# Kernel optimization log

Measured on AMD Instinct MI355X. Metric: run time of the kernel, lower is better.

Reference implementation:

```python
import jax, jax.numpy as jnp
import numpy as np

DIM = 768
HEADS = 12
HEAD_DIM = DIM // HEADS
SCALE = HEAD_DIM ** -0.5
EPS = 1e-6


def setup_inputs() -> dict:
    key = jax.random.key(0)
    ks = jax.random.split(key, 10)
    B, Nq, Nk, C = 4, 4096, 4096, DIM
    std = C ** -0.5
    return {
        "x_q": jax.random.normal(ks[0], (B, Nq, C), jnp.float32),
        "x_kv": jax.random.normal(ks[1], (B, Nk, C), jnp.float32),
        "Wq": jax.random.normal(ks[2], (C, C), jnp.float32) * std,
        "bq": jnp.zeros((C,), jnp.float32),
        "Wk": jax.random.normal(ks[3], (C, C), jnp.float32) * std,
        "bk": jnp.zeros((C,), jnp.float32),
        "Wv": jax.random.normal(ks[4], (C, C), jnp.float32) * std,
        "bv": jnp.zeros((C,), jnp.float32),
        "Wp": jax.random.normal(ks[5], (C, C), jnp.float32) * std,
        "bp": jnp.zeros((C,), jnp.float32),
    }


def _phi(x):
    # ELU(alpha=1) + 1 positive feature map
    return jax.nn.elu(x) + 1.0


def reference(x_q, x_kv, Wq, bq, Wk, bk, Wv, bv, Wp, bp):
    B, Nq, C = x_q.shape
    Nk = x_kv.shape[1]
    h, d = HEADS, HEAD_DIM
    # projections (torch Linear: x @ W.T + b)
    q = x_q @ Wq.T + bq   # [B,Nq,C]
    k = x_kv @ Wk.T + bk  # [B,Nk,C]
    v = x_kv @ Wv.T + bv  # [B,Nk,C]
    # split heads -> [B,h,N,d]
    q = q.reshape(B, Nq, h, d).transpose(0, 2, 1, 3) * SCALE
    k = k.reshape(B, Nk, h, d).transpose(0, 2, 1, 3)
    v = v.reshape(B, Nk, h, d).transpose(0, 2, 1, 3)
    q_phi = _phi(q)
    k_phi = _phi(k)
    # KV state [B,h,d,d] and normalizer sum [B,h,d]
    kv = jnp.einsum('bhnd,bhne->bhde', k_phi, v)
    k_sum = k_phi.sum(axis=2)
    out = jnp.einsum('bhnd,bhde->bhne', q_phi, kv)
    z = jnp.einsum('bhnd,bhd->bhn', q_phi, k_sum)[..., None] + EPS
    out = out / z
    out = out.transpose(0, 2, 1, 3).reshape(B, Nq, C)
    return out @ Wp.T + bp
```

## Files before the change

### kernel.cpp

```cpp
#include <hip/hip_runtime.h>
#include <hip/hip_bf16.h>
#include <cstdint>
#include <cstddef>

#define HD_B   4
#define SEQ    4096
#define CDIM   768
#define HEADS  12
#define HDIM   64
#define MROWS  (HD_B * SEQ)
#define QSCALE 0.125f
#define EPSV   1e-6f

typedef __attribute__((ext_vector_type(8))) short  short8v;
typedef __attribute__((ext_vector_type(4))) float  f32x4;

__device__ __forceinline__ unsigned short f2b(float f) {
    unsigned int u = __float_as_uint(f);
    u += 0x7FFFu + ((u >> 16) & 1u);
    return (unsigned short)(u >> 16);
}
__device__ __forceinline__ float b2f(unsigned short b) {
    return __uint_as_float(((unsigned int)b) << 16);
}
__device__ __forceinline__ float phi_f(float x) {
    return x > 0.f ? x + 1.f : __expf(x);
}

#define GLOAD_LDS16(g, l)                                             \
    __builtin_amdgcn_global_load_lds(                                 \
        (__attribute__((address_space(1))) void*)(void*)(g),          \
        (__attribute__((address_space(3))) void*)(l), 16, 0, 0)

#define VMW12() asm volatile("s_waitcnt vmcnt(12)" ::: "memory")
#define VMW4()  asm volatile("s_waitcnt vmcnt(4)"  ::: "memory")
#define VMW0()  asm volatile("s_waitcnt vmcnt(0)"  ::: "memory")
#define LGW()   asm volatile("s_waitcnt lgkmcnt(0)" ::: "memory")
#define SB()    do { __builtin_amdgcn_sched_barrier(0);               \
                     __builtin_amdgcn_s_barrier();                    \
                     __builtin_amdgcn_sched_barrier(0); } while (0)

__global__ void wcvt_all(const float* __restrict__ wq, const float* __restrict__ wk,
                         const float* __restrict__ wv, const float* __restrict__ wp,
                         unsigned short* __restrict__ dst) {
    const int y = blockIdx.y;
    const float* src = (y == 0) ? wq : (y == 1) ? wk : (y == 2) ? wv : wp;
    const int i = blockIdx.x * 256 + threadIdx.x;
    float4 v = reinterpret_cast<const float4*>(src)[i];
    ushort4 o;
    o.x = f2b(v.x); o.y = f2b(v.y); o.z = f2b(v.z); o.w = f2b(v.w);
    reinterpret_cast<ushort4*>(dst + (size_t)y * (CDIM * CDIM))[i] = o;
}

template <int EPI, int NC>
__device__ __forceinline__ void proj_body(
    const float* __restrict__ A32,
    const unsigned short* __restrict__ Bp,
    const float* __restrict__ b0, const float* __restrict__ b1,
    unsigned short* __restrict__ o0, unsigned short* __restrict__ o1)
{
    constexpr int K  = CDIM;
    constexpr int T  = NC * 128;
    constexpr int NT = K / 64;

    __shared__ __align__(16) char smem[49152];
    char* As = smem;

    const int tid  = threadIdx.x;
    const int lane = tid & 63;
    const int w    = tid >> 6;
    const int wr   = w >> 1, wc = w & 1;

    const int bid  = blockIdx.x;
    const int s    = (bid & 7) * (T >> 3) + (bid >> 3);
    const int colp = s % NC;
    const int rowp = s / NC;
    const int brow = rowp * 128;
    const int bcol = colp * 128;

    const int r8  = lane >> 3;
    const int c8e = ((lane & 7) ^ r8) << 3;
    const int ar  = lane >> 4;
    const int ac  = (lane & 15) << 2;
    const int fr  = lane & 15;
    const int hi4 = lane >> 4;

    f32x4 acc[4][4];
#pragma unroll
    for (int i = 0; i < 4; ++i)
#pragma unroll
        for (int j = 0; j < 4; ++j)
            acc[i][j] = (f32x4){0.f, 0.f, 0.f, 0.f};

    auto stageB = [&](int buf, int kt) {
        char* dst = smem + 16384 + buf * 16384;
#pragma unroll
        for (int g = 0; g < 4; ++g) {
            const unsigned short* src =
                Bp + (size_t)(bcol + w * 32 + g * 8 + r8) * K + kt * 64 + c8e;
            GLOAD_LDS16(src, dst + (w * 32 + g * 8) * 128);
        }
    };

    float4 fA[8];
    auto aload = [&](int kt) {
#pragma unroll
        for (int j = 0; j < 8; ++j)
            fA[j] = *(const float4*)(A32 + (size_t)(brow + w * 32 + j * 4 + ar) * K
                                     + kt * 64 + ac);
    };
    auto awrite = [&]() {
#pragma unroll
        for (int j = 0; j < 8; ++j) {
            const int row = w * 32 + j * 4 + ar;
            unsigned int p0, p1;
            asm("v_cvt_pk_bf16_f32 %0, %1, %2" : "=v"(p0) : "v"(fA[j].x), "v"(fA[j].y));
            asm("v_cvt_pk_bf16_f32 %0, %1, %2" : "=v"(p1) : "v"(fA[j].z), "v"(fA[j].w));
            uint2 pk; pk.x = p0; pk.y = p1;
            *(uint2*)(As + row * 128 + ((ac << 1) ^ ((row & 7) << 4))) = pk;
        }
    };
    auto compute = [&](int bbuf) {
        const char* Bb = smem + 16384 + bbuf * 16384;
        short8v a[4][2];
#pragma unroll
        for (int i = 0; i < 4; ++i) {
            const int row = wr * 64 + i * 16 + fr;
#pragma unroll
            for (int ks = 0; ks < 2; ++ks)
                a[i][ks] = *(const short8v*)(As + row * 128 +
                              ((((ks << 2) + hi4) ^ (row & 7)) << 4));
        }
#pragma unroll
        for (int j = 0; j < 4; ++j) {
            const int row = wc * 64 + j * 16 + fr;
            short8v bb0 = *(const short8v*)(Bb + row * 128 + ((hi4 ^ (row & 7)) << 4));
            short8v bb1 = *(const short8v*)(Bb + row * 128 + (((4 + hi4) ^ (row & 7)) << 4));
#pragma unroll
            for (int i = 0; i < 4; ++i) {
                acc[i][j] = __builtin_amdgcn_mfma_f32_16x16x32_bf16(a[i][0], bb0, acc[i][j], 0, 0, 0);
                acc[i][j] = __builtin_amdgcn_mfma_f32_16x16x32_bf16(a[i][1], bb1, acc[i][j], 0, 0, 0);
            }
        }
    };

    aload(0);
    stageB(0, 0);
    VMW4();
    awrite();
    aload(1);
    stageB(1, 1);
    LGW();
    SB();

    for (int t = 0; t < NT; ++t) {
        const int c = t & 1;
        if (t == NT - 1) { VMW0(); } else { VMW12(); }
        SB();
        compute(c);
        SB();
        if (t < NT - 1) {
            VMW4();
            awrite();
            if (t < NT - 2) { aload(t + 2); stageB(c, t + 2); }
            LGW();
        }
    }

    float* ep = (float*)(void*)smem + w * (16 * 68);
    const int rr = lane >> 2;
    const int cb = (lane & 3) * 4;
    const bool isV = (EPI == 1) && (colp >= 6);
    const float* bptr = (EPI == 0) ? (b0 + bcol)
                        : (isV ? (b1 + (bcol - 768)) : (b0 + bcol));
    const int colbase = ((EPI == 1 && isV) ? bcol - 768 : bcol) + wc * 64;
    unsigned short* o16 = (EPI == 1 && isV) ? o1 : o0;

    float4 bb[4];
#pragma unroll
    for (int q = 0; q < 4; ++q)
        bb[q] = *(const float4*)&bptr[wc * 64 + q * 16 + cb];

#pragma unroll
    for (int i = 0; i < 4; ++i) {
#pragma unroll
        for (int j = 0; j < 4; ++j)
#pragma unroll
            for (int r = 0; r < 4; ++r)
                ep[(hi4 * 4 + r) * 68 + j * 16 + fr] = acc[i][j][r];
#pragma unroll
        for (int q = 0; q < 4; ++q) {
            const int cc = q * 16 + cb;
            f32x4 v = *(const f32x4*)&ep[rr * 68 + cc];
            const int rg = brow + wr * 64 + i * 16 + rr;
            const float4 bq = bb[q];
            ushort4 ov;
            if (EPI == 0) {
                ov.x = f2b(phi_f((v[0] + bq.x) * QSCALE));
                ov.y = f2b(phi_f((v[1] + bq.y) * QSCALE));
                ov.z = f2b(phi_f((v[2] + bq.z) * QSCALE));
                ov.w = f2b(phi_f((v[3] + bq.w) * QSCALE));
            } else if (!isV) {
                ov.x = f2b(phi_f(v[0] + bq.x));
                ov.y = f2b(phi_f(v[1] + bq.y));
                ov.z = f2b(phi_f(v[2] + bq.z));
                ov.w = f2b(phi_f(v[3] + bq.w));
            } else {
                ov.x = f2b(v[0] + bq.x);
                ov.y = f2b(v[1] + bq.y);
                ov.z = f2b(v[2] + bq.z);
                ov.w = f2b(v[3] + bq.w);
            }
            *(ushort4*)(o16 + (size_t)rg * 768 + (colbase + cc)) = ov;
        }
    }
}

__global__ __launch_bounds__(256, 3) void g_q(
    const float* __restrict__ xq, const unsigned short* __restrict__ wq,
    const float* __restrict__ bq, unsigned short* __restrict__ qphi)
{
    proj_body<0, 6>(xq, wq, bq, nullptr, qphi, nullptr);
}

__global__ __launch_bounds__(256, 3) void g_kv(
    const float* __restrict__ xkv, const unsigned short* __restrict__ wkv,
    const float* __restrict__ bk, const float* __restrict__ bv,
    unsigned short* __restrict__ kphi, unsigned short* __restrict__ v16)
{
    proj_body<1, 12>(xkv, wkv, bk, bv, kphi, v16);
}

__global__ __launch_bounds__(256) void g_out(
    const unsigned short* __restrict__ A16,
    const unsigned short* __restrict__ Bp,
    const float* __restrict__ bias,
    float* __restrict__ outp)
{
    constexpr int K = CDIM;
    __shared__ __align__(16) char smem[32768];
    char* As = smem;
    char* Bs = smem + 16384;

    const int tid  = threadIdx.x;
    const int lane = tid & 63;
    const int w    = tid >> 6;
    const int wr   = w >> 1, wc = w & 1;
    const int brow = blockIdx.x * 128;
    const int bcol = blockIdx.y * 128;

    const int r8  = lane >> 3;
    const int c8e = ((lane & 7) ^ r8) << 3;
    const int fr  = lane & 15;
    const int hi4 = lane >> 4;

    f32x4 acc[4][4];
#pragma unroll
    for (int i = 0; i < 4; ++i)
#pragma unroll
        for (int j = 0; j < 4; ++j)
            acc[i][j] = (f32x4){0.f, 0.f, 0.f, 0.f};

    for (int k0 = 0; k0 < K; k0 += 64) {
#pragma unroll
        for (int g = 0; g < 4; ++g) {
            const unsigned short* srcA =
                A16 + (size_t)(brow + w * 32 + g * 8 + r8) * K + k0 + c8e;
            GLOAD_LDS16(srcA, As + (w * 32 + g * 8) * 128);
            const unsigned short* srcB =
                Bp + (size_t)(bcol + w * 32 + g * 8 + r8) * K + k0 + c8e;
            GLOAD_LDS16(srcB, Bs + (w * 32 + g * 8) * 128);
        }
        __syncthreads();

        short8v a[4][2], b[4][2];
#pragma unroll
        for (int i = 0; i < 4; ++i) {
            const int row = wr * 64 + i * 16 + fr;
#pragma unroll
            for (int ks = 0; ks < 2; ++ks)
                a[i][ks] = *(const short8v*)(As + row * 128 +
                              ((((ks << 2) + hi4) ^ (row & 7)) << 4));
        }
#pragma unroll
        for (int j = 0; j < 4; ++j) {
            const int row = wc * 64 + j * 16 + fr;
#pragma unroll
            for (int ks = 0; ks < 2; ++ks)
                b[j][ks] = *(const short8v*)(Bs + row * 128 +
                              ((((ks << 2) + hi4) ^ (row & 7)) << 4));
        }
#pragma unroll
        for (int i = 0; i < 4; ++i)
#pragma unroll
            for (int j = 0; j < 4; ++j) {
                acc[i][j] = __builtin_amdgcn_mfma_f32_16x16x32_bf16(a[i][0], b[j][0], acc[i][j], 0, 0, 0);
                acc[i][j] = __builtin_amdgcn_mfma_f32_16x16x32_bf16(a[i][1], b[j][1], acc[i][j], 0, 0, 0);
            }
        __syncthreads();
    }

    float* ep = (float*)(void*)smem + w * (16 * 68);
    const int rr = lane >> 2;
    const int cb = (lane & 3) * 4;
    float4 bb[4];
#pragma unroll
    for (int q = 0; q < 4; ++q)
        bb[q] = *(const float4*)&bias[bcol + wc * 64 + q * 16 + cb];
#pragma unroll
    for (int i = 0; i < 4; ++i) {
#pragma unroll
        for (int j = 0; j < 4; ++j)
#pragma unroll
            for (int r = 0; r < 4; ++r)
                ep[(hi4 * 4 + r) * 68 + j * 16 + fr] = acc[i][j][r];
#pragma unroll
        for (int q = 0; q < 4; ++q) {
            const int cc = q * 16 + cb;
            f32x4 v = *(const f32x4*)&ep[rr * 68 + cc];
            const int rg = brow + wr * 64 + i * 16 + rr;
            const int cg = bcol + wc * 64 + cc;
            const float4 bq = bb[q];
            float4 ov;
            ov.x = v[0] + bq.x; ov.y = v[1] + bq.y;
            ov.z = v[2] + bq.z; ov.w = v[3] + bq.w;
            *(float4*)(outp + (size_t)rg * 768 + cg) = ov;
        }
    }
}

#define KVCH   128
#define KVITER 2
#define NCHUNK 16

__global__ __launch_bounds__(256, 3) void kv_part(
    const unsigned short* __restrict__ kphi,
    const unsigned short* __restrict__ vmat,
    float* __restrict__ part)
{
    const int bh = blockIdx.y;
    const int b  = bh / HEADS, h = bh % HEADS;
    const int c  = blockIdx.x;
    __shared__ unsigned short Kl[KVCH][HDIM];
    __shared__ float Vl[KVCH][HDIM];
    const int t  = threadIdx.x;
    const int i  = t >> 2;
    const int jb = t & 3;

    float acc[16];
#pragma unroll
    for (int jj = 0; jj < 16; ++jj) acc[jj] = 0.f;
    float ksum = 0.f;

    for (int it = 0; it < KVITER; ++it) {
        const size_t rbase = (size_t)b * SEQ + (size_t)c * (KVCH * KVITER) + it * KVCH;
        __syncthreads();
        for (int l = 0; l < KVCH / 32; ++l) {
            int row = l * 32 + (t >> 3);
            int col = (t & 7) << 3;
            const size_t g = (rbase + row) * CDIM + h * HDIM + col;
            int4 kk = *(const int4*)(kphi + g);
            int4 vv = *(const int4*)(vmat + g);
            *(int4*)&Kl[row][col] = kk;
            const unsigned short* vp = (const unsigned short*)&vv;
            float4 lo, hi;
            lo.x = b2f(vp[0]); lo.y = b2f(vp[1]); lo.z = b2f(vp[2]); lo.w = b2f(vp[3]);
            hi.x = b2f(vp[4]); hi.y = b2f(vp[5]); hi.z = b2f(vp[6]); hi.w = b2f(vp[7]);
            *(float4*)&Vl[row][col]     = lo;
            *(float4*)&Vl[row][col + 4] = hi;
        }
        __syncthreads();
        for (int n = 0; n < KVCH; ++n) {
            float kf = b2f(Kl[n][i]);
            const float4* vr = (const float4*)&Vl[n][jb * 16];
            float4 v0 = vr[0], v1 = vr[1], v2 = vr[2], v3 = vr[3];
            acc[0]  += kf * v0.x; acc[1]  += kf * v0.y; acc[2]  += kf * v0.z; acc[3]  += kf * v0.w;
            acc[4]  += kf * v1.x; acc[5]  += kf * v1.y; acc[6]  += kf * v1.z; acc[7]  += kf * v1.w;
            acc[8]  += kf * v2.x; acc[9]  += kf * v2.y; acc[10] += kf * v2.z; acc[11] += kf * v2.w;
            acc[12] += kf * v3.x; acc[13] += kf * v3.y; acc[14] += kf * v3.z; acc[15] += kf * v3.w;
            ksum += kf;
        }
    }
    float* op = part + ((size_t)c * 48 + bh) * 4160;
#pragma unroll
    for (int jj = 0; jj < 16; ++jj) op[i * 64 + jb * 16 + jj] = acc[jj];
    if (jb == 0) op[4096 + i] = ksum;
}

__global__ void kv_finalize(const float* __restrict__ part, float* __restrict__ kv) {
    int idx = blockIdx.x * 256 + threadIdx.x;
    if (idx >= 48 * 4160) return;
    float s = 0.f;
    for (int c = 0; c < NCHUNK; ++c) s += part[(size_t)c * 48 * 4160 + idx];
    kv[idx] = s;
}

__global__ __launch_bounds__(256) void attn_apply(
    const unsigned short* __restrict__ qphi,
    const float* __restrict__ kv,
    unsigned short* __restrict__ attn)
{
    const int h  = blockIdx.y;
    const int m0 = blockIdx.x * 64;
    const int b  = m0 >> 12;
    const int bh = b * HEADS + h;
    __shared__ float kvs[HDIM][HDIM];
    __shared__ float ksums[HDIM];
    __shared__ unsigned short ql[64][HDIM];
    const int t = threadIdx.x;
    const float* kvp = kv + (size_t)bh * 4160;
#pragma unroll
    for (int it = 0; it < 4; ++it) {
        int e = it * 1024 + t * 4;
        *(float4*)&kvs[e >> 6][e & 63] = *(const float4*)&kvp[e];
    }
    if (t < 64) ksums[t] = kvp[4096 + t];
#pragma unroll
    for (int it = 0; it < 2; ++it) {
        int row = it * 32 + (t >> 3);
        int col = (t & 7) << 3;
        *(int4*)&ql[row][col] =
            *(const int4*)(qphi + (size_t)(m0 + row) * CDIM + h * HDIM + col);
    }
    __syncthreads();

    const int r  = t >> 2;
    const int jb = t & 3;
    float acc[16];
#pragma unroll
    for (int jj = 0; jj < 16; ++jj) acc[jj] = 0.f;
    float z = 0.f;
    for (int q8 = 0; q8 < 8; ++q8) {
        short8v qv = *(const short8v*)&ql[r][q8 * 8];
#pragma unroll
        for (int dd = 0; dd < 8; ++dd) {
            float qd = b2f((unsigned short)qv[dd]);
            int d = q8 * 8 + dd;
            const float4* kr = (const float4*)&kvs[d][jb * 16];
            float4 k0 = kr[0], k1 = kr[1], k2 = kr[2], k3 = kr[3];
            acc[0]  += qd * k0.x; acc[1]  += qd * k0.y; acc[2]  += qd * k0.z; acc[3]  += qd * k0.w;
            acc[4]  += qd * k1.x; acc[5]  += qd * k1.y; acc[6]  += qd * k1.z; acc[7]  += qd * k1.w;
            acc[8]  += qd * k2.x; acc[9]  += qd * k2.y; acc[10] += qd * k2.z; acc[11] += qd * k2.w;
            acc[12] += qd * k3.x; acc[13] += qd * k3.y; acc[14] += qd * k3.z; acc[15] += qd * k3.w;
            z += qd * ksums[d];
        }
    }
    const float inv = 1.f / (z + EPSV);
    unsigned short* op = attn + (size_t)(m0 + r) * CDIM + h * HDIM + jb * 16;
#pragma unroll
    for (int jj = 0; jj < 16; ++jj) op[jj] = f2b(acc[jj] * inv);
}

extern "C" void kernel_launch(void* const* d_in, const int* in_sizes, int n_in,
                              void* d_out, int out_size, void* d_ws, size_t ws_size,
                              hipStream_t stream)
{
    const float* x_q  = (const float*)d_in[0];
    const float* x_kv = (const float*)d_in[1];
    const float* Wq   = (const float*)d_in[2];
    const float* bq   = (const float*)d_in[3];
    const float* Wk   = (const float*)d_in[4];
    const float* bk   = (const float*)d_in[5];
    const float* Wv   = (const float*)d_in[6];
    const float* bv   = (const float*)d_in[7];
    const float* Wp   = (const float*)d_in[8];
    const float* bp   = (const float*)d_in[9];
    float* out = (float*)d_out;

    char* ws = (char*)d_ws;
    size_t off = 0;
    auto alloc = [&](size_t bytes) -> char* {
        char* p = ws + off;
        off += (bytes + 255) & ~(size_t)255;
        return p;
    };
    const size_t xelems = (size_t)MROWS * CDIM;
    const size_t welems = (size_t)CDIM * CDIM;

    unsigned short* w16    = (unsigned short*)alloc(4 * welems * 2);
    unsigned short* wkv16  = w16 + welems;
    unsigned short* wp16   = w16 + 3 * welems;
    unsigned short* qphi   = (unsigned short*)alloc(xelems * 2);
    unsigned short* kphi   = (unsigned short*)alloc(xelems * 2);
    unsigned short* v16    = (unsigned short*)alloc(xelems * 2);
    unsigned short* attn16 = (unsigned short*)alloc(xelems * 2);
    float* part = (float*)alloc((size_t)NCHUNK * 48 * 4160 * 4);
    float* kvf  = (float*)alloc((size_t)48 * 4160 * 4);

    wcvt_all<<<dim3(576, 4), 256, 0, stream>>>(Wq, Wk, Wv, Wp, w16);

    g_q<<<768, 256, 0, stream>>>(x_q, w16, bq, qphi);

    g_kv<<<1536, 256, 0, stream>>>(x_kv, wkv16, bk, bv, kphi, v16);

    kv_part<<<dim3(NCHUNK, 48), 256, 0, stream>>>(kphi, v16, part);
    kv_finalize<<<(48 * 4160 + 255) / 256, 256, 0, stream>>>(part, kvf);
    attn_apply<<<dim3(MROWS / 64, HEADS), 256, 0, stream>>>(qphi, kvf, attn16);

    g_out<<<dim3(128, 6), 256, 0, stream>>>(attn16, wp16, bp, out);
}
```

Before: 214.0 us.

## Merge Q and KV projections into one launch and double-buffer output GEMM

The separate Q and KV projection kernels are replaced by one g_qkv kernel with 18 column tiles per row block, which picks the input, weight slice, bias and epilogue per tile from the column index. This removes a kernel launch and the tail between the two projections. The output projection GEMM gets a double-buffered LDS pipeline with global_load_lds prefetch two tiles ahead and vmcnt waits, instead of a load-sync-compute loop. It also gets the same bid-swizzled 1D grid mapping. LDS for g_out grows to 64KB, which may lower occupancy, and the merged kernel adds runtime branching on mode.

```diff
diff --git a/kernel.cpp b/kernel.cpp
--- a/kernel.cpp
+++ b/kernel.cpp
@@ -33,6 +33,7 @@
         (__attribute__((address_space(3))) void*)(l), 16, 0, 0)
 
 #define VMW12() asm volatile("s_waitcnt vmcnt(12)" ::: "memory")
+#define VMW8()  asm volatile("s_waitcnt vmcnt(8)"  ::: "memory")
 #define VMW4()  asm volatile("s_waitcnt vmcnt(4)"  ::: "memory")
 #define VMW0()  asm volatile("s_waitcnt vmcnt(0)"  ::: "memory")
 #define LGW()   asm volatile("s_waitcnt lgkmcnt(0)" ::: "memory")
@@ -52,14 +53,17 @@
     reinterpret_cast<ushort4*>(dst + (size_t)y * (CDIM * CDIM))[i] = o;
 }
 
-template <int EPI, int NC>
-__device__ __forceinline__ void proj_body(
-    const float* __restrict__ A32,
-    const unsigned short* __restrict__ Bp,
+__global__ __launch_bounds__(256, 3) void g_qkv(
+    const float* __restrict__ Aq,
+    const float* __restrict__ Akv,
+    const unsigned short* __restrict__ Wb,
     const float* __restrict__ b0, const float* __restrict__ b1,
-    unsigned short* __restrict__ o0, unsigned short* __restrict__ o1)
+    const float* __restrict__ b2,
+    unsigned short* __restrict__ out_q, unsigned short* __restrict__ out_k,
+    unsigned short* __restrict__ out_v)
 {
     constexpr int K  = CDIM;
+    constexpr int NC = 18;
     constexpr int T  = NC * 128;
     constexpr int NT = K / 64;
 
@@ -76,7 +80,11 @@
     const int colp = s % NC;
     const int rowp = s / NC;
     const int brow = rowp * 128;
-    const int bcol = colp * 128;
+    const int mode = colp / 6;
+    const int bcol = (colp % 6) * 128;
+
+    const float* A32 = (mode == 0) ? Aq : Akv;
+    const unsigned short* Bp = Wb + (size_t)mode * (K * K);
 
     const int r8  = lane >> 3;
     const int c8e = ((lane & 7) ^ r8) << 3;
@@ -170,11 +178,8 @@
     float* ep = (float*)(void*)smem + w * (16 * 68);
     const int rr = lane >> 2;
     const int cb = (lane & 3) * 4;
-    const bool isV = (EPI == 1) && (colp >= 6);
-    const float* bptr = (EPI == 0) ? (b0 + bcol)
-                        : (isV ? (b1 + (bcol - 768)) : (b0 + bcol));
-    const int colbase = ((EPI == 1 && isV) ? bcol - 768 : bcol) + wc * 64;
-    unsigned short* o16 = (EPI == 1 && isV) ? o1 : o0;
+    const float* bptr = (mode == 0 ? b0 : (mode == 1 ? b1 : b2)) + bcol;
+    unsigned short* o16 = (mode == 0 ? out_q : (mode == 1 ? out_k : out_v));
 
     float4 bb[4];
 #pragma unroll
@@ -193,14 +198,15 @@
             const int cc = q * 16 + cb;
             f32x4 v = *(const f32x4*)&ep[rr * 68 + cc];
             const int rg = brow + wr * 64 + i * 16 + rr;
+            const int cg = bcol + wc * 64 + cc;
             const float4 bq = bb[q];
             ushort4 ov;
-            if (EPI == 0) {
+            if (mode == 0) {
                 ov.x = f2b(phi_f((v[0] + bq.x) * QSCALE));
                 ov.y = f2b(phi_f((v[1] + bq.y) * QSCALE));
                 ov.z = f2b(phi_f((v[2] + bq.z) * QSCALE));
                 ov.w = f2b(phi_f((v[3] + bq.w) * QSCALE));
-            } else if (!isV) {
+            } else if (mode == 1) {
                 ov.x = f2b(phi_f(v[0] + bq.x));
                 ov.y = f2b(phi_f(v[1] + bq.y));
                 ov.z = f2b(phi_f(v[2] + bq.z));
@@ -211,24 +217,9 @@
                 ov.z = f2b(v[2] + bq.z);
                 ov.w = f2b(v[3] + bq.w);
             }
-            *(ushort4*)(o16 + (size_t)rg * 768 + (colbase + cc)) = ov;
-        }
-    }
-}
-
-__global__ __launch_bounds__(256, 3) void g_q(
-    const float* __restrict__ xq, const unsigned short* __restrict__ wq,
-    const float* __restrict__ bq, unsigned short* __restrict__ qphi)
-{
-    proj_body<0, 6>(xq, wq, bq, nullptr, qphi, nullptr);
-}
-
-__global__ __launch_bounds__(256, 3) void g_kv(
-    const float* __restrict__ xkv, const unsigned short* __restrict__ wkv,
-    const float* __restrict__ bk, const float* __restrict__ bv,
-    unsigned short* __restrict__ kphi, unsigned short* __restrict__ v16)
-{
-    proj_body<1, 12>(xkv, wkv, bk, bv, kphi, v16);
+            *(ushort4*)(o16 + (size_t)rg * 768 + cg) = ov;
+        }
+    }
 }
 
 __global__ __launch_bounds__(256) void g_out(
@@ -237,17 +228,21 @@
     const float* __restrict__ bias,
     float* __restrict__ outp)
 {
-    constexpr int K = CDIM;
-    __shared__ __align__(16) char smem[32768];
-    char* As = smem;
-    char* Bs = smem + 16384;
+    constexpr int K  = CDIM;
+    constexpr int NT = K / 64;
+    __shared__ __align__(16) char smem[65536];
 
     const int tid  = threadIdx.x;
     const int lane = tid & 63;
     const int w    = tid >> 6;
     const int wr   = w >> 1, wc = w & 1;
-    const int brow = blockIdx.x * 128;
-    const int bcol = blockIdx.y * 128;
+
+    const int bid  = blockIdx.x;
+    const int s    = (bid & 7) * (768 >> 3) + (bid >> 3);
+    const int colp = s % 6;
+    const int rowp = s / 6;
+    const int brow = rowp * 128;
+    const int bcol = colp * 128;
 
     const int r8  = lane >> 3;
     const int c8e = ((lane & 7) ^ r8) << 3;
@@ -261,25 +256,34 @@
         for (int j = 0; j < 4; ++j)
             acc[i][j] = (f32x4){0.f, 0.f, 0.f, 0.f};
 
-    for (int k0 = 0; k0 < K; k0 += 64) {
+    auto stageA = [&](int buf, int kt) {
+        char* dst = smem + buf * 16384;
 #pragma unroll
         for (int g = 0; g < 4; ++g) {
-            const unsigned short* srcA =
-                A16 + (size_t)(brow + w * 32 + g * 8 + r8) * K + k0 + c8e;
-            GLOAD_LDS16(srcA, As + (w * 32 + g * 8) * 128);
-            const unsigned short* srcB =
-                Bp + (size_t)(bcol + w * 32 + g * 8 + r8) * K + k0 + c8e;
-            GLOAD_LDS16(srcB, Bs + (w * 32 + g * 8) * 128);
-        }
-        __syncthreads();
-
+            const unsigned short* src =
+                A16 + (size_t)(brow + w * 32 + g * 8 + r8) * K + kt * 64 + c8e;
+            GLOAD_LDS16(src, dst + (w * 32 + g * 8) * 128);
+        }
+    };
+    auto stageB = [&](int buf, int kt) {
+        char* dst = smem + 32768 + buf * 16384;
+#pragma unroll
+        for (int g = 0; g < 4; ++g) {
+            const unsigned short* src =
+                Bp + (size_t)(bcol + w * 32 + g * 8 + r8) * K + kt * 64 + c8e;
+            GLOAD_LDS16(src, dst + (w * 32 + g * 8) * 128);
+        }
+    };
+    auto compute = [&](int buf) {
+        const char* Ab = smem + buf * 16384;
+        const char* Bb = smem + 32768 + buf * 16384;
         short8v a[4][2], b[4][2];
 #pragma unroll
         for (int i = 0; i < 4; ++i) {
             const int row = wr * 64 + i * 16 + fr;
 #pragma unroll
             for (int ks = 0; ks < 2; ++ks)
-                a[i][ks] = *(const short8v*)(As + row * 128 +
+                a[i][ks] = *(const short8v*)(Ab + row * 128 +
                               ((((ks << 2) + hi4) ^ (row & 7)) << 4));
         }
 #pragma unroll
@@ -287,7 +291,7 @@
             const int row = wc * 64 + j * 16 + fr;
 #pragma unroll
             for (int ks = 0; ks < 2; ++ks)
-                b[j][ks] = *(const short8v*)(Bs + row * 128 +
+                b[j][ks] = *(const short8v*)(Bb + row * 128 +
                               ((((ks << 2) + hi4) ^ (row & 7)) << 4));
         }
 #pragma unroll
@@ -297,7 +301,17 @@
                 acc[i][j] = __builtin_amdgcn_mfma_f32_16x16x32_bf16(a[i][0], b[j][0], acc[i][j], 0, 0, 0);
                 acc[i][j] = __builtin_amdgcn_mfma_f32_16x16x32_bf16(a[i][1], b[j][1], acc[i][j], 0, 0, 0);
             }
-        __syncthreads();
+    };
+
+    stageA(0, 0); stageB(0, 0);
+    stageA(1, 1); stageB(1, 1);
+    for (int t = 0; t < NT; ++t) {
+        const int c = t & 1;
+        if (t == NT - 1) { VMW0(); } else { VMW8(); }
+        SB();
+        compute(c);
+        SB();
+        if (t < NT - 2) { stageA(c, t + 2); stageB(c, t + 2); }
     }
 
     float* ep = (float*)(void*)smem + w * (16 * 68);
@@ -478,7 +492,6 @@
     const size_t welems = (size_t)CDIM * CDIM;
 
     unsigned short* w16    = (unsigned short*)alloc(4 * welems * 2);
-    unsigned short* wkv16  = w16 + welems;
     unsigned short* wp16   = w16 + 3 * welems;
     unsigned short* qphi   = (unsigned short*)alloc(xelems * 2);
     unsigned short* kphi   = (unsigned short*)alloc(xelems * 2);
@@ -489,13 +502,11 @@
 
     wcvt_all<<<dim3(576, 4), 256, 0, stream>>>(Wq, Wk, Wv, Wp, w16);
 
-    g_q<<<768, 256, 0, stream>>>(x_q, w16, bq, qphi);
-
-    g_kv<<<1536, 256, 0, stream>>>(x_kv, wkv16, bk, bv, kphi, v16);
+    g_qkv<<<2304, 256, 0, stream>>>(x_q, x_kv, w16, bq, bk, bv, qphi, kphi, v16);
 
     kv_part<<<dim3(NCHUNK, 48), 256, 0, stream>>>(kphi, v16, part);
     kv_finalize<<<(48 * 4160 + 255) / 256, 256, 0, stream>>>(part, kvf);
     attn_apply<<<dim3(MROWS / 64, HEADS), 256, 0, stream>>>(qphi, kvf, attn16);
 
-    g_out<<<dim3(128, 6), 256, 0, stream>>>(attn16, wp16, bp, out);
-}
+    g_out<<<768, 256, 0, stream>>>(attn16, wp16, bp, out);
+}
```

After: 205.7 us. 1.04x faster.
